# Performance work log

Measured on AMD Instinct MI355X. Metric: run time of the kernel, lower is better.

Reference implementation:

```python
import jax, jax.numpy as jnp
import numpy as np

N_NODES = 100000
N_EDGES = 1000000
D = 128  # latent_dim


def setup_inputs() -> dict:
    key = jax.random.key(0)
    ks = jax.random.split(key, 8)
    z = jax.random.normal(ks[0], (N_NODES, D), dtype=jnp.float32)
    edge_index = jax.random.randint(ks[1], (2, N_EDGES), 0, N_NODES, dtype=jnp.int64)
    # MLP params: Linear(2D->D), Linear(D->D//2), Linear(D//2->1)
    def lin(k, fan_in, fan_out):
        kw, kb = jax.random.split(k)
        bound = 1.0 / np.sqrt(fan_in)
        W = jax.random.uniform(kw, (fan_in, fan_out), jnp.float32, -bound, bound)
        b = jax.random.uniform(kb, (fan_out,), jnp.float32, -bound, bound)
        return W, b
    W1, b1 = lin(ks[2], 2 * D, D)
    W2, b2 = lin(ks[3], D, D // 2)
    W3, b3 = lin(ks[4], D // 2, 1)
    return {"z": z, "edge_index": edge_index, "W1": W1, "b1": b1,
            "W2": W2, "b2": b2, "W3": W3, "b3": b3}


def reference(z, edge_index, W1, b1, W2, b2, W3, b3):
    # Gather src/dst node embeddings and concat: [E, 2D]
    h = jnp.concatenate([z[edge_index[0]], z[edge_index[1]]], axis=-1)
    h = jax.nn.relu(h @ W1 + b1)      # [E, D]
    h = jax.nn.relu(h @ W2 + b2)      # [E, D//2]
    out = h @ W3 + b3                 # [E, 1]
    return out  # sigmoid=False default
```

## Files before the change

kernel.cpp:

```cpp
#include <hip/hip_runtime.h>
#include <hip/hip_bf16.h>
#include <string.h>

#define NE 1000000
#define NN 100000
#define NWT 31250
#define NGT2 3125

typedef __attribute__((ext_vector_type(8))) short bf16x8;
typedef __attribute__((ext_vector_type(4))) float f32x4;

__device__ __forceinline__ unsigned short f2bf(float f) {
  unsigned u = __builtin_bit_cast(unsigned, f);
  u += 0x7fffu + ((u >> 16) & 1u);
  return (unsigned short)(u >> 16);
}
__device__ __forceinline__ unsigned pk2(float a, float b) {
  __hip_bfloat162 h = __float22bfloat162_rn(make_float2(a, b));
  unsigned r;
  memcpy(&r, &h, 4);
  return r;
}
__device__ __forceinline__ float lo2f(unsigned u) {
  return __builtin_bit_cast(float, u << 16);
}
__device__ __forceinline__ float hi2f(unsigned u) {
  return __builtin_bit_cast(float, u & 0xffff0000u);
}

__global__ void prep(const float* __restrict__ W1, const float* __restrict__ W2,
                     unsigned short* __restrict__ afw, unsigned short* __restrict__ fw2) {
  int tid = blockIdx.x * 256 + threadIdx.x;
  if (tid < 32768) {
    int j = tid & 7, l = (tid >> 3) & 63, kb = (tid >> 9) & 3, mt = tid >> 11;
    int k = kb * 32 + (l >> 4) * 8 + j;
    int n = mt * 16 + (l & 15);
    float v = (n < 128) ? W1[k * 128 + n] : W1[(128 + k) * 128 + (n - 128)];
    afw[tid] = f2bf(v);
  } else if (tid < 40960) {
    int t = tid - 32768;
    int j = t & 7, l = (t >> 3) & 63, kb = (t >> 9) & 3, nt = t >> 11;
    fw2[t] = f2bf(W2[(kb * 32 + (l >> 4) * 8 + j) * 64 + nt * 16 + (l & 15)]);
  }
}

__global__ __launch_bounds__(256, 2) void node_gemm(
    const float* __restrict__ z, const unsigned short* __restrict__ afw,
    const float* __restrict__ b1, unsigned short* __restrict__ h1ab) {
  __shared__ __align__(16) bf16x8 sfw[4096];
  {
    const int t = threadIdx.x;
#pragma unroll
    for (int it = 0; it < 16; it++)
      sfw[it * 256 + t] = ((const bf16x8*)afw)[it * 256 + t];
  }
  __syncthreads();

  const int l = threadIdx.x & 63, w = threadIdx.x >> 6;
  const int wt = blockIdx.x * 4 + w;
  if (wt >= NGT2) return;
  const int c = l & 15, g = l >> 4;
  const int n0 = wt * 32;

  uint4 zlb[2][4];
#pragma unroll
  for (int grp = 0; grp < 2; grp++)
#pragma unroll
    for (int kb = 0; kb < 4; kb++) {
      const float* zp = z + (n0 + grp * 16 + c) * 128 + kb * 32 + g * 8;
      float4 a = *(const float4*)zp;
      float4 b = *(const float4*)(zp + 4);
      zlb[grp][kb] = (uint4){pk2(a.x, a.y), pk2(a.z, a.w), pk2(b.x, b.y), pk2(b.z, b.w)};
    }

  f32x4 acc[2][16] = {};
#pragma unroll
  for (int kb = 0; kb < 4; kb++) {
    bf16x8 bf0 = __builtin_bit_cast(bf16x8, zlb[0][kb]);
    bf16x8 bf1 = __builtin_bit_cast(bf16x8, zlb[1][kb]);
#pragma unroll
    for (int mt = 0; mt < 16; mt++) {
      bf16x8 af = sfw[(mt * 4 + kb) * 64 + l];
      acc[0][mt] = __builtin_amdgcn_mfma_f32_16x16x32_bf16(af, bf0, acc[0][mt], 0, 0, 0);
      acc[1][mt] = __builtin_amdgcn_mfma_f32_16x16x32_bf16(af, bf1, acc[1][mt], 0, 0, 0);
    }
  }

#pragma unroll
  for (int grp = 0; grp < 2; grp++)
#pragma unroll
    for (int mt = 0; mt < 16; mt++) {
      const int f0 = mt * 16 + g * 4;
      float v0 = acc[grp][mt][0], v1 = acc[grp][mt][1];
      float v2 = acc[grp][mt][2], v3 = acc[grp][mt][3];
      if (mt < 8) {
        float4 bb = *(const float4*)(b1 + f0);
        v0 += bb.x; v1 += bb.y; v2 += bb.z; v3 += bb.w;
      }
      uint2 pk = {pk2(v0, v1), pk2(v2, v3)};
      *(uint2*)(h1ab + (n0 + grp * 16 + c) * 256 + f0) = pk;
    }
}

__global__ __launch_bounds__(256, 6) void mlp_edge(
    const unsigned short* __restrict__ h1ab, const int* __restrict__ edge,
    const unsigned short* __restrict__ fw2,
    const float* __restrict__ b2, const float* __restrict__ W3,
    const float* __restrict__ b3, float* __restrict__ out) {
  __shared__ __align__(16) unsigned short sfw2[8192];
  {
    const int t = threadIdx.x;
#pragma unroll
    for (int st = 0; st < 4; st++)
      ((bf16x8*)sfw2)[st * 256 + t] = ((const bf16x8*)fw2)[st * 256 + t];
  }
  __syncthreads();

  const int l = threadIdx.x & 63, w = threadIdx.x >> 6;
  const int wt = blockIdx.x * 4 + w;
  if (wt >= NWT) return;
  const int c = l & 15, g = l >> 4;
  const int eBase = wt * 32;

  const char* hb = (const char*)h1ab;
  const unsigned kbase = (unsigned)g * 16u;

  const int e0 = eBase + c;
  const unsigned so0 = (unsigned)edge[e0] * 512u + kbase;
  const unsigned so1 = (unsigned)edge[e0 + 16] * 512u + kbase;
  const unsigned do0 = (unsigned)edge[NE + e0] * 512u + 256u + kbase;
  const unsigned do1 = (unsigned)edge[NE + e0 + 16] * 512u + 256u + kbase;

  f32x4 acc2[2][4] = {};
#pragma unroll
  for (int kb = 0; kb < 4; kb++) {
    const unsigned o = (unsigned)kb * 64u;
    uint4 sv[2], dv[2];
    sv[0] = *(const uint4*)(hb + so0 + o);
    sv[1] = *(const uint4*)(hb + so1 + o);
    dv[0] = *(const uint4*)(hb + do0 + o);
    dv[1] = *(const uint4*)(hb + do1 + o);

    bf16x8 a2[2];
#pragma unroll
    for (int mt = 0; mt < 2; mt++) {
      uint4 s = sv[mt], d = dv[mt];
      uint4 r;
      r.x = pk2(fmaxf(lo2f(s.x) + lo2f(d.x), 0.f), fmaxf(hi2f(s.x) + hi2f(d.x), 0.f));
      r.y = pk2(fmaxf(lo2f(s.y) + lo2f(d.y), 0.f), fmaxf(hi2f(s.y) + hi2f(d.y), 0.f));
      r.z = pk2(fmaxf(lo2f(s.z) + lo2f(d.z), 0.f), fmaxf(hi2f(s.z) + hi2f(d.z), 0.f));
      r.w = pk2(fmaxf(lo2f(s.w) + lo2f(d.w), 0.f), fmaxf(hi2f(s.w) + hi2f(d.w), 0.f));
      a2[mt] = __builtin_bit_cast(bf16x8, r);
    }
#pragma unroll
    for (int nt = 0; nt < 4; nt++) {
      bf16x8 bf = ((const bf16x8*)sfw2)[(nt * 4 + kb) * 64 + l];
      acc2[0][nt] = __builtin_amdgcn_mfma_f32_16x16x32_bf16(a2[0], bf, acc2[0][nt], 0, 0, 0);
      acc2[1][nt] = __builtin_amdgcn_mfma_f32_16x16x32_bf16(a2[1], bf, acc2[1][nt], 0, 0, 0);
    }
  }

  float w3v[4], b2v[4];
#pragma unroll
  for (int nt = 0; nt < 4; nt++) {
    w3v[nt] = W3[nt * 16 + c];
    b2v[nt] = b2[nt * 16 + c];
  }
  const float bias3 = b3[0];
#pragma unroll
  for (int mt = 0; mt < 2; mt++) {
#pragma unroll
    for (int i = 0; i < 4; i++) {
      float t = 0.f;
#pragma unroll
      for (int nt = 0; nt < 4; nt++)
        t += fmaxf(acc2[mt][nt][i] + b2v[nt], 0.f) * w3v[nt];
      t += __shfl_xor(t, 1);
      t += __shfl_xor(t, 2);
      t += __shfl_xor(t, 4);
      t += __shfl_xor(t, 8);
      if (c == 0) out[eBase + mt * 16 + g * 4 + i] = t + bias3;
    }
  }
}

extern "C" void kernel_launch(void* const* d_in, const int* in_sizes, int n_in,
                              void* d_out, int out_size, void* d_ws, size_t ws_size,
                              hipStream_t stream) {
  const float* z  = (const float*)d_in[0];
  const int* edge = (const int*)d_in[1];
  const float* W1 = (const float*)d_in[2];
  const float* b1 = (const float*)d_in[3];
  const float* W2 = (const float*)d_in[4];
  const float* b2 = (const float*)d_in[5];
  const float* W3 = (const float*)d_in[6];
  const float* b3 = (const float*)d_in[7];
  float* out = (float*)d_out;

  unsigned short* afw  = (unsigned short*)d_ws;
  unsigned short* fw2  = afw + 32768;
  unsigned short* h1ab = fw2 + 8192;

  prep<<<160, 256, 0, stream>>>(W1, W2, afw, fw2);
  node_gemm<<<(NGT2 + 3) / 4, 256, 0, stream>>>(z, afw, b1, h1ab);
  mlp_edge<<<(NWT + 3) / 4, 256, 0, stream>>>(h1ab, edge, fw2, b2, W3, b3, out);
}
```

Measured before the change: 200.8 us.

## Split node GEMM across feature halves and drop LDS weight staging

The node GEMM now assigns 16 nodes per wave and splits the 256 output features between two waves. Each wave reads its W1 fragments straight from global memory (L2-cached) instead of staging the full 64 KB weight matrix in LDS, and occupancy is raised to 4 blocks. This removes the per-block LDS fill and syncthreads and shrinks the accumulator register footprint, at the cost of redundant global weight reads and z being loaded twice per node. The edge kernel also switches the edge-index loads and output stores to nontemporal hints.

```diff
diff --git a/kernel.cpp b/kernel.cpp
--- a/kernel.cpp
+++ b/kernel.cpp
@@ -5,7 +5,7 @@
 #define NE 1000000
 #define NN 100000
 #define NWT 31250
-#define NGT2 3125
+#define NGT 6250
 
 typedef __attribute__((ext_vector_type(8))) short bf16x8;
 typedef __attribute__((ext_vector_type(4))) float f32x4;
@@ -44,62 +44,47 @@
   }
 }
 
-__global__ __launch_bounds__(256, 2) void node_gemm(
+__global__ __launch_bounds__(256, 4) void node_gemm(
     const float* __restrict__ z, const unsigned short* __restrict__ afw,
     const float* __restrict__ b1, unsigned short* __restrict__ h1ab) {
-  __shared__ __align__(16) bf16x8 sfw[4096];
-  {
-    const int t = threadIdx.x;
-#pragma unroll
-    for (int it = 0; it < 16; it++)
-      sfw[it * 256 + t] = ((const bf16x8*)afw)[it * 256 + t];
-  }
-  __syncthreads();
+  const int l = threadIdx.x & 63, w = threadIdx.x >> 6;
+  const int nh = w >> 1, fh = w & 1;
+  const int wt = blockIdx.x * 2 + nh;
+  if (wt >= NGT) return;
+  const int c = l & 15, g = l >> 4;
+  const int n0 = wt * 16;
 
-  const int l = threadIdx.x & 63, w = threadIdx.x >> 6;
-  const int wt = blockIdx.x * 4 + w;
-  if (wt >= NGT2) return;
-  const int c = l & 15, g = l >> 4;
-  const int n0 = wt * 32;
-
-  uint4 zlb[2][4];
-#pragma unroll
-  for (int grp = 0; grp < 2; grp++)
-#pragma unroll
-    for (int kb = 0; kb < 4; kb++) {
-      const float* zp = z + (n0 + grp * 16 + c) * 128 + kb * 32 + g * 8;
-      float4 a = *(const float4*)zp;
-      float4 b = *(const float4*)(zp + 4);
-      zlb[grp][kb] = (uint4){pk2(a.x, a.y), pk2(a.z, a.w), pk2(b.x, b.y), pk2(b.z, b.w)};
-    }
-
-  f32x4 acc[2][16] = {};
+  uint4 zlb[4];
 #pragma unroll
   for (int kb = 0; kb < 4; kb++) {
-    bf16x8 bf0 = __builtin_bit_cast(bf16x8, zlb[0][kb]);
-    bf16x8 bf1 = __builtin_bit_cast(bf16x8, zlb[1][kb]);
+    const float* zp = z + (n0 + c) * 128 + kb * 32 + g * 8;
+    float4 a = *(const float4*)zp;
+    float4 b = *(const float4*)(zp + 4);
+    zlb[kb] = (uint4){pk2(a.x, a.y), pk2(a.z, a.w), pk2(b.x, b.y), pk2(b.z, b.w)};
+  }
+
+  f32x4 acc[8] = {};
 #pragma unroll
-    for (int mt = 0; mt < 16; mt++) {
-      bf16x8 af = sfw[(mt * 4 + kb) * 64 + l];
-      acc[0][mt] = __builtin_amdgcn_mfma_f32_16x16x32_bf16(af, bf0, acc[0][mt], 0, 0, 0);
-      acc[1][mt] = __builtin_amdgcn_mfma_f32_16x16x32_bf16(af, bf1, acc[1][mt], 0, 0, 0);
+  for (int kb = 0; kb < 4; kb++) {
+    bf16x8 bfrag = __builtin_bit_cast(bf16x8, zlb[kb]);
+#pragma unroll
+    for (int mt = 0; mt < 8; mt++) {
+      bf16x8 af = *(const bf16x8*)(afw + (((fh * 8 + mt) * 4 + kb) * 64 + l) * 8);
+      acc[mt] = __builtin_amdgcn_mfma_f32_16x16x32_bf16(af, bfrag, acc[mt], 0, 0, 0);
     }
   }
 
 #pragma unroll
-  for (int grp = 0; grp < 2; grp++)
-#pragma unroll
-    for (int mt = 0; mt < 16; mt++) {
-      const int f0 = mt * 16 + g * 4;
-      float v0 = acc[grp][mt][0], v1 = acc[grp][mt][1];
-      float v2 = acc[grp][mt][2], v3 = acc[grp][mt][3];
-      if (mt < 8) {
-        float4 bb = *(const float4*)(b1 + f0);
-        v0 += bb.x; v1 += bb.y; v2 += bb.z; v3 += bb.w;
-      }
-      uint2 pk = {pk2(v0, v1), pk2(v2, v3)};
-      *(uint2*)(h1ab + (n0 + grp * 16 + c) * 256 + f0) = pk;
+  for (int mt = 0; mt < 8; mt++) {
+    const int f0 = (fh * 8 + mt) * 16 + g * 4;
+    float v0 = acc[mt][0], v1 = acc[mt][1], v2 = acc[mt][2], v3 = acc[mt][3];
+    if (fh == 0) {
+      float4 bb = *(const float4*)(b1 + f0);
+      v0 += bb.x; v1 += bb.y; v2 += bb.z; v3 += bb.w;
     }
+    uint2 pk = {pk2(v0, v1), pk2(v2, v3)};
+    *(uint2*)(h1ab + (n0 + c) * 256 + f0) = pk;
+  }
 }
 
 __global__ __launch_bounds__(256, 6) void mlp_edge(
@@ -126,10 +111,14 @@
   const unsigned kbase = (unsigned)g * 16u;
 
   const int e0 = eBase + c;
-  const unsigned so0 = (unsigned)edge[e0] * 512u + kbase;
-  const unsigned so1 = (unsigned)edge[e0 + 16] * 512u + kbase;
-  const unsigned do0 = (unsigned)edge[NE + e0] * 512u + 256u + kbase;
-  const unsigned do1 = (unsigned)edge[NE + e0 + 16] * 512u + 256u + kbase;
+  const int is0 = __builtin_nontemporal_load(edge + e0);
+  const int is1 = __builtin_nontemporal_load(edge + e0 + 16);
+  const int id0 = __builtin_nontemporal_load(edge + NE + e0);
+  const int id1 = __builtin_nontemporal_load(edge + NE + e0 + 16);
+  const unsigned so0 = (unsigned)is0 * 512u + kbase;
+  const unsigned so1 = (unsigned)is1 * 512u + kbase;
+  const unsigned do0 = (unsigned)id0 * 512u + 256u + kbase;
+  const unsigned do1 = (unsigned)id1 * 512u + 256u + kbase;
 
   f32x4 acc2[2][4] = {};
 #pragma unroll
@@ -179,7 +168,8 @@
       t += __shfl_xor(t, 2);
       t += __shfl_xor(t, 4);
       t += __shfl_xor(t, 8);
-      if (c == 0) out[eBase + mt * 16 + g * 4 + i] = t + bias3;
+      if (c == 0)
+        __builtin_nontemporal_store(t + bias3, out + eBase + mt * 16 + g * 4 + i);
     }
   }
 }
@@ -202,6 +192,6 @@
   unsigned short* h1ab = fw2 + 8192;
 
   prep<<<160, 256, 0, stream>>>(W1, W2, afw, fw2);
-  node_gemm<<<(NGT2 + 3) / 4, 256, 0, stream>>>(z, afw, b1, h1ab);
+  node_gemm<<<NGT / 2, 256, 0, stream>>>(z, afw, b1, h1ab);
   mlp_edge<<<(NWT + 3) / 4, 256, 0, stream>>>(h1ab, edge, fw2, b2, W3, b3, out);
 }
```

New measurement: 214.7 us. +6.9%, slower.
